# Performance work log

Hardware: AMD Instinct MI355X
Metric: run time of the kernel (lower is better)

The kernel has to match this reference:

```python
import jax, jax.numpy as jnp
import numpy as np


def setup_inputs() -> dict:
    key = jax.random.key(0)
    k1, k2 = jax.random.split(key)
    batch, cw_dim = 4096, 1024
    dim_embedding, book_size = 8, 256
    dim_codes = cw_dim // dim_embedding  # 128
    x = jax.random.normal(k1, (batch, cw_dim), dtype=jnp.float32)
    codebook = jax.random.normal(k2, (dim_codes, book_size, dim_embedding), dtype=jnp.float32)
    return {"x": x, "codebook": codebook}


def reference(x, codebook):
    # Faithful JAX version of VQVAE.quantise:
    #   pairwise squared distance -> argmin -> gather embeddings -> one-hot scatter
    C, K, D = codebook.shape          # dim_codes, book_size, dim_embedding
    B = x.shape[0]
    xr = x.reshape(B, C, D)           # [B, C, D] (= view(batch*dim_codes, 1, D))
    x2 = jnp.sum(xr * xr, axis=-1)                       # [B, C]
    c2 = jnp.sum(codebook * codebook, axis=-1)           # [C, K]
    dist = x2[..., None] - 2.0 * jnp.einsum('bcd,ckd->bck', xr, codebook) + c2[None]
    idx = jnp.argmin(dist, axis=-1)                      # [B, C]
    # gather nearest codebook entry per code slot
    cw_embed = codebook[jnp.arange(C)[None, :], idx]     # [B, C, D]
    cw_embed = cw_embed.reshape(B, C * D)                # [B, cw_dim]
    # one-hot scatter of selected indices
    one_hot_idx = jax.nn.one_hot(idx, K, dtype=jnp.float32)  # [B, C, K]
    return cw_embed, one_hot_idx
```

## Files before the change

### kernel.cpp

```cpp
#include <hip/hip_runtime.h>


constexpr int B_  = 4096;
constexpr int C_  = 128;
constexpr int K_  = 256;
constexpr int D_  = 8;
constexpr int TPB = 256;

constexpr int   BPT   = 4;
constexpr int   BTILE = TPB * BPT;
constexpr float TAU2  = 1.0e-3f;

typedef float vf4 __attribute__((ext_vector_type(4)));

__global__ __launch_bounds__(TPB) void vq_fused(
    const float* __restrict__ x,
    const float* __restrict__ cb,
    float* __restrict__ out_embed,
    float* __restrict__ out_onehot)
{
    __shared__ float s_cbf[K_ * D_];
    __shared__ float s_c2f[K_];

    const int c    = blockIdx.x;
    const int bt   = blockIdx.y;
    const int tid  = threadIdx.x;
    const int lane = tid & 63;
    const int wave = tid >> 6;

    {
        const float4* gcb = (const float4*)(cb + (size_t)c * (K_ * D_));
        ((float4*)s_cbf)[tid]       = gcb[tid];
        ((float4*)s_cbf)[tid + TPB] = gcb[tid + TPB];
    }
    __syncthreads();
    {
        const float* v = s_cbf + tid * D_;
        float s = 0.f;
        #pragma unroll
        for (int d = 0; d < D_; ++d) s = fmaf(v[d], v[d], s);
        s_c2f[tid] = s;
    }
    __syncthreads();

    const float4* scb4 = (const float4*)s_cbf;
    const int bbase = bt * BTILE;

    float xf[BPT][D_];
    #pragma unroll
    for (int j = 0; j < BPT; ++j) {
        const int b = bbase + j * TPB + tid;
        const float4* xp = (const float4*)(x + (size_t)b * (C_ * D_) + c * D_);
        const float4 a = xp[0];
        const float4 h = xp[1];
        xf[j][0] = a.x; xf[j][1] = a.y; xf[j][2] = a.z; xf[j][3] = a.w;
        xf[j][4] = h.x; xf[j][5] = h.y; xf[j][6] = h.z; xf[j][7] = h.w;
    }

    float s1[BPT], s2[BPT];
    int   k1[BPT];
    #pragma unroll
    for (int j = 0; j < BPT; ++j) { s1[j] = 3.4e38f; s2[j] = 3.4e38f; k1[j] = 0; }

    #pragma unroll 2
    for (int k = 0; k < K_; ++k) {
        const float4 clo = scb4[k * 2];
        const float4 chi = scb4[k * 2 + 1];
        const float  c2k = s_c2f[k];
        #pragma unroll
        for (int j = 0; j < BPT; ++j) {
            float dot = xf[j][0] * clo.x;
            dot = fmaf(xf[j][1], clo.y, dot);
            dot = fmaf(xf[j][2], clo.z, dot);
            dot = fmaf(xf[j][3], clo.w, dot);
            dot = fmaf(xf[j][4], chi.x, dot);
            dot = fmaf(xf[j][5], chi.y, dot);
            dot = fmaf(xf[j][6], chi.z, dot);
            dot = fmaf(xf[j][7], chi.w, dot);
            const float score = fmaf(-2.f, dot, c2k);
            s2[j] = fminf(s2[j], fmaxf(score, s1[j]));
            const bool lt = score < s1[j];
            k1[j] = lt ? k : k1[j];
            s1[j] = lt ? score : s1[j];
        }
    }

    #pragma unroll
    for (int j = 0; j < BPT; ++j) {
        const bool amb = (s2[j] - s1[j]) <= TAU2;
        unsigned long long mask = __ballot(amb);
        while (mask) {
            const int src = (int)__ffsll((long long)mask) - 1;
            mask &= mask - 1;
            double xd[D_];
            #pragma unroll
            for (int d = 0; d < D_; ++d) xd[d] = (double)__shfl(xf[j][d], src);
            double best = 1.0e300;
            int    bk   = 0;
            #pragma unroll
            for (int t = 0; t < 4; ++t) {
                const int k = lane * 4 + t;
                const float* cv = s_cbf + k * D_;
                double cd[D_];
                #pragma unroll
                for (int d = 0; d < D_; ++d) cd[d] = (double)cv[d];
                double c2k = 0.0;
                #pragma unroll
                for (int d = 0; d < D_; ++d) c2k = fma(cd[d], cd[d], c2k);
                double dot = xd[0] * cd[0];
                #pragma unroll
                for (int d = 1; d < D_; ++d) dot = fma(xd[d], cd[d], dot);
                const double score = fma(-2.0, dot, c2k);
                if (score < best) { best = score; bk = k; }
            }
            #pragma unroll
            for (int off = 32; off >= 1; off >>= 1) {
                const double ob  = __shfl_down(best, off);
                const int    obk = __shfl_down(bk,   off);
                if (ob < best) { best = ob; bk = obk; }
            }
            const int win = __shfl(bk, 0);
            if (lane == src) k1[j] = win;
        }
    }

    #pragma unroll
    for (int j = 0; j < BPT; ++j) {
        const int    b    = bbase + j * TPB + tid;
        const size_t pair = (size_t)b * C_ + c;
        float4* dst = (float4*)(out_embed + pair * D_);
        dst[0] = ((const float4*)s_cbf)[k1[j] * 2];
        dst[1] = ((const float4*)s_cbf)[k1[j] * 2 + 1];

        const int bw = bbase + j * TPB + wave * 64;
        const int e0 = lane * 4;
        #pragma unroll 8
        for (int i = 0; i < 64; ++i) {
            const int k = __builtin_amdgcn_readlane(k1[j], i);
            vf4 v;
            v.x = (k == e0    ) ? 1.f : 0.f;
            v.y = (k == e0 + 1) ? 1.f : 0.f;
            v.z = (k == e0 + 2) ? 1.f : 0.f;
            v.w = (k == e0 + 3) ? 1.f : 0.f;
            const size_t row = (size_t)(bw + i) * C_ + c;
            ((vf4*)(out_onehot + row * K_))[lane] = v;
        }
    }
}

extern "C" void kernel_launch(void* const* d_in, const int* in_sizes, int n_in,
                              void* d_out, int out_size, void* d_ws, size_t ws_size,
                              hipStream_t stream) {
    const float* x  = (const float*)d_in[0];
    const float* cb = (const float*)d_in[1];
    float* out        = (float*)d_out;
    float* out_embed  = out;
    float* out_onehot = out + (size_t)B_ * C_ * D_;

    dim3 grid(C_, B_ / BTILE);
    vq_fused<<<grid, TPB, 0, stream>>>(x, cb, out_embed, out_onehot);
}
```

Baseline: 594.5 us.

## Split argmin and output writing into two kernels via index workspace

Splits the fused kernel in two. The first kernel computes the nearest-code index and stores it to a workspace. The second kernel writes the one-hot rows and gathered embeddings in row-major order, so each block covers contiguous output regions. The old one-hot writes were strided by C across rows within a codebook column, and the new layout aims to make writes coalesced and sequential. The cost is an extra kernel launch, an index round trip through global memory, and gathered codebook reads from global memory.

After: 604.9 us. About the same (+1.7%).

```diff
diff --git a/kernel.cpp b/kernel.cpp
--- a/kernel.cpp
+++ b/kernel.cpp
@@ -6,6 +6,7 @@
 constexpr int K_  = 256;
 constexpr int D_  = 8;
 constexpr int TPB = 256;
+constexpr int NP  = B_ * C_;
 
 constexpr int   BPT   = 4;
 constexpr int   BTILE = TPB * BPT;
@@ -13,11 +14,10 @@
 
 typedef float vf4 __attribute__((ext_vector_type(4)));
 
-__global__ __launch_bounds__(TPB) void vq_fused(
+__global__ __launch_bounds__(TPB) void vq_screen_fix(
     const float* __restrict__ x,
     const float* __restrict__ cb,
-    float* __restrict__ out_embed,
-    float* __restrict__ out_onehot)
+    int* __restrict__ idx_out)
 {
     __shared__ float s_cbf[K_ * D_];
     __shared__ float s_c2f[K_];
@@ -26,7 +26,6 @@
     const int bt   = blockIdx.y;
     const int tid  = threadIdx.x;
     const int lane = tid & 63;
-    const int wave = tid >> 6;
 
     {
         const float4* gcb = (const float4*)(cb + (size_t)c * (K_ * D_));
@@ -126,25 +125,50 @@
 
     #pragma unroll
     for (int j = 0; j < BPT; ++j) {
-        const int    b    = bbase + j * TPB + tid;
-        const size_t pair = (size_t)b * C_ + c;
-        float4* dst = (float4*)(out_embed + pair * D_);
-        dst[0] = ((const float4*)s_cbf)[k1[j] * 2];
-        dst[1] = ((const float4*)s_cbf)[k1[j] * 2 + 1];
+        const int b = bbase + j * TPB + tid;
+        idx_out[(size_t)b * C_ + c] = k1[j];
+    }
+}
 
-        const int bw = bbase + j * TPB + wave * 64;
-        const int e0 = lane * 4;
-        #pragma unroll 8
-        for (int i = 0; i < 64; ++i) {
-            const int k = __builtin_amdgcn_readlane(k1[j], i);
-            vf4 v;
-            v.x = (k == e0    ) ? 1.f : 0.f;
-            v.y = (k == e0 + 1) ? 1.f : 0.f;
-            v.z = (k == e0 + 2) ? 1.f : 0.f;
-            v.w = (k == e0 + 3) ? 1.f : 0.f;
-            const size_t row = (size_t)(bw + i) * C_ + c;
-            ((vf4*)(out_onehot + row * K_))[lane] = v;
-        }
+constexpr int GRID2 = 2048;
+constexpr int RPB   = NP / GRID2;
+
+__global__ __launch_bounds__(TPB, 4) void vq_write(
+    const int*   __restrict__ idx,
+    const float* __restrict__ cb,
+    float* __restrict__ out_embed,
+    float* __restrict__ out_onehot)
+{
+    const int tid  = threadIdx.x;
+    const int lane = tid & 63;
+    const int wave = tid >> 6;
+    const int blk  = blockIdx.x;
+
+    const int rowbase = blk * RPB + wave * 64;
+    const int myk = idx[rowbase + lane];
+    const int e0 = lane * 4;
+    #pragma unroll 8
+    for (int i = 0; i < 64; ++i) {
+        const int k = __builtin_amdgcn_readlane(myk, i);
+        vf4 v;
+        v.x = (k == e0    ) ? 1.f : 0.f;
+        v.y = (k == e0 + 1) ? 1.f : 0.f;
+        v.z = (k == e0 + 2) ? 1.f : 0.f;
+        v.w = (k == e0 + 3) ? 1.f : 0.f;
+        ((vf4*)(out_onehot + (size_t)(rowbase + i) * K_))[lane] = v;
+    }
+
+    const size_t pbase = (size_t)blk * RPB;
+    #pragma unroll
+    for (int i = 0; i < 2; ++i) {
+        const int    f    = i * TPB + tid;
+        const int    pl   = f >> 1;
+        const int    half = f & 1;
+        const size_t pair = pbase + pl;
+        const int    c    = (int)(pair & (C_ - 1));
+        const int    k    = idx[pair];
+        const vf4 val = ((const vf4*)(cb + ((size_t)c * K_ + k) * D_))[half];
+        ((vf4*)(out_embed + pbase * D_))[f] = val;
     }
 }
 
@@ -156,7 +180,10 @@
     float* out        = (float*)d_out;
     float* out_embed  = out;
     float* out_onehot = out + (size_t)B_ * C_ * D_;
+    int*   idx_ws     = (int*)d_ws;
 
-    dim3 grid(C_, B_ / BTILE);
-    vq_fused<<<grid, TPB, 0, stream>>>(x, cb, out_embed, out_onehot);
+    dim3 grid1(C_, B_ / BTILE);
+    vq_screen_fix<<<grid1, TPB, 0, stream>>>(x, cb, idx_ws);
+
+    vq_write<<<GRID2, TPB, 0, stream>>>(idx_ws, cb, out_embed, out_onehot);
 }
```
